# Kernel tuning notes

Hardware: AMD Instinct MI355X
Metric: run time of the kernel (lower is better)

## Reference

```python
import jax, jax.numpy as jnp
import numpy as np

B, L, K1, P = 16, 224, 8192, 16  # batch, spectral bands, pixels, endmembers
LEAKY_SLOPE = 0.01  # torch nn.LeakyReLU default


def setup_inputs() -> dict:
    key = jax.random.key(0)
    ks = jax.random.split(key, 7)
    return {
        "a": jax.random.normal(ks[0], (B, P, K1), jnp.float32),
        "d2": jax.random.normal(ks[1], (B, P, K1), jnp.float32),
        "y": jax.random.normal(ks[2], (B, L, K1), jnp.float32),
        "w3_w": jax.random.normal(ks[3], (P, P), jnp.float32) * 0.1,  # Conv1d(P,P,1) weight squeezed
        "b3_w": jax.random.normal(ks[4], (P, P), jnp.float32) * 0.1,
        "w3_c": jax.random.normal(ks[5], (1, L, P), jnp.float32),     # kernel codebook
        "sigma": jnp.ones((1,), jnp.float32) * 2.0,
        "ca_w": jax.random.normal(ks[6], (2, P), jnp.float32) * 0.1,  # CA Conv1d(P,2,1) weight squeezed
    }


def reference(a, d2, y, w3_w, b3_w, w3_c, sigma, ca_w):
    # h2 = Conv1d(P,P,1)(a - d2)  -> pointwise matmul over channel dim
    h2 = jnp.einsum('pq,bqn->bpn', w3_w, a - d2)  # (B,P,K1)

    # GaussianKernelLayer: pairwise L2 distances between y pixels (B,L,K1)
    # and codebook columns w3_c (1,L,P), via the GEMM identity
    # ||u-v||^2 = ||u||^2 + ||v||^2 - 2 u.v  (avoids the (B,L,K1,P) broadcast).
    y_sq = jnp.sum(y * y, axis=1)            # (B,K1)
    c_sq = jnp.sum(w3_c * w3_c, axis=1)      # (1,P)
    cross = jnp.einsum('blk,olp->bkp', y, w3_c)  # (B,K1,P)
    dist_sq = jnp.maximum(y_sq[:, :, None] + c_sq[:, None, :] - 2.0 * cross, 0.0)
    dist = jnp.sqrt(dist_sq)                 # (B,K1,P)
    h3 = jnp.exp(-0.5 * jnp.square(dist / sigma[0]))
    h3 = jnp.transpose(h3, (0, 2, 1))        # (B,P,K1)

    # CA channel attention: avg/max pool over pixels -> Conv1d(P,2,1) -> LeakyReLU -> softmax
    avg = jnp.mean(h3, axis=-1)              # (B,P)
    mx = jnp.max(h3, axis=-1)                # (B,P)
    conv_lrelu = lambda v: jax.nn.leaky_relu(jnp.einsum('cp,bp->bc', ca_w, v), LEAKY_SLOPE)
    ratio = jax.nn.softmax(conv_lrelu(avg) + conv_lrelu(mx), axis=-1)  # (B,2)

    # combine center pixel + mean pixel via bmm with ratio
    mid = h3[:, :, K1 // 2]                  # (B,P)
    mean = jnp.mean(h3, axis=-1)             # (B,P)
    stacked = jnp.stack([mid, mean], axis=1)  # (B,2,P)
    comb = jnp.einsum('bc,bcp->bp', ratio, stacked)  # (B,P)

    # h4 = Conv1d(P,P,1)(comb[:, :, None])
    h4 = jnp.einsum('pq,bq->bp', b3_w, comb)[:, :, None]  # (B,P,1)

    return h4 + h2  # broadcast over pixel dim -> (B,P,K1)
```

## Files before the change

### kernel.cpp

```cpp
#include <hip/hip_runtime.h>

#define Bn  16
#define Ln  224
#define K1n 8192
#define Pn  16
#define NCHUNK 32


__global__ __launch_bounds__(256) void k_stats(
    const float* __restrict__ y,
    const float* __restrict__ w3c,
    const float* __restrict__ sigma,
    float* __restrict__ ws_sum,
    float* __restrict__ ws_max,
    float* __restrict__ ws_mid)
{
    __shared__ float s_csq_part[16][Pn];
    __shared__ float s_csq[Pn];
    __shared__ float s_part_s[4][Pn];
    __shared__ float s_part_m[4][Pn];

    const int tid   = threadIdx.x;
    const int b     = blockIdx.x >> 5;
    const int chunk = blockIdx.x & 31;
    const int k     = (chunk << 8) + tid;

    {
        const int p   = tid & 15;
        const int sub = tid >> 4;
        float cs = 0.f;
#pragma unroll
        for (int l = sub; l < Ln; l += 16) {
            float v = w3c[l * Pn + p];
            cs = fmaf(v, v, cs);
        }
        s_csq_part[sub][p] = cs;
    }
    __syncthreads();
    if (tid < Pn) {
        float cs = 0.f;
#pragma unroll
        for (int s = 0; s < 16; ++s) cs += s_csq_part[s][tid];
        s_csq[tid] = cs;
    }
    __syncthreads();

    float cross[Pn];
#pragma unroll
    for (int p = 0; p < Pn; ++p) cross[p] = 0.f;
    float ysq = 0.f;

    const float* yp = y + (size_t)b * Ln * K1n + k;
#pragma unroll 16
    for (int l = 0; l < Ln; ++l) {
        float v = yp[(size_t)l * K1n];
        ysq = fmaf(v, v, ysq);
        const float* wrow = w3c + l * Pn;
#pragma unroll
        for (int p = 0; p < Pn; ++p) cross[p] = fmaf(v, wrow[p], cross[p]);
    }

    const float sg = sigma[0];
    const float nh = -0.5f / (sg * sg);

    float h3[Pn];
#pragma unroll
    for (int p = 0; p < Pn; ++p) {
        float d = fmaxf(ysq + s_csq[p] - 2.f * cross[p], 0.f);
        h3[p] = __expf(d * nh);
    }

    if (k == (K1n / 2)) {
#pragma unroll
        for (int p = 0; p < Pn; ++p) ws_mid[b * Pn + p] = h3[p];
    }

    const int lane = tid & 63;
    const int wv   = tid >> 6;
#pragma unroll
    for (int p = 0; p < Pn; ++p) {
        float s = h3[p];
        float m = h3[p];
#pragma unroll
        for (int off = 32; off > 0; off >>= 1) {
            s += __shfl_down(s, off, 64);
            m = fmaxf(m, __shfl_down(m, off, 64));
        }
        if (lane == 0) { s_part_s[wv][p] = s; s_part_m[wv][p] = m; }
    }
    __syncthreads();
    if (tid < Pn) {
        float s = s_part_s[0][tid] + s_part_s[1][tid] + s_part_s[2][tid] + s_part_s[3][tid];
        float m = fmaxf(fmaxf(s_part_m[0][tid], s_part_m[1][tid]),
                        fmaxf(s_part_m[2][tid], s_part_m[3][tid]));
        const int base = (b * NCHUNK + chunk) * Pn + tid;
        ws_sum[base] = s;
        ws_max[base] = m;
    }
}

__global__ __launch_bounds__(256) void k_out(
    const float* __restrict__ a,
    const float* __restrict__ d2,
    const float* __restrict__ w3w,
    const float* __restrict__ b3w,
    const float* __restrict__ caw,
    const float* __restrict__ ws_sum,
    const float* __restrict__ ws_max,
    const float* __restrict__ ws_mid,
    float* __restrict__ out)
{
    __shared__ float s_w3w[Pn][Pn];
    __shared__ float s_red_s[16][Pn];
    __shared__ float s_red_m[16][Pn];
    __shared__ float s_avg[Pn], s_mx[Pn], s_mid[Pn], s_comb[Pn], s_h4[Pn];
    __shared__ float s_t[2];

    const int tid = threadIdx.x;
    const int b   = blockIdx.x >> 5;
    const int k   = ((blockIdx.x & 31) << 8) + tid;

    if (tid < Pn * Pn) s_w3w[tid >> 4][tid & 15] = w3w[tid];

    {
        const int p   = tid & 15;
        const int grp = tid >> 4;
        const int i0  = (b * NCHUNK + grp)      * Pn + p;
        const int i1  = (b * NCHUNK + grp + 16) * Pn + p;
        if (grp < 16) {
            s_red_s[grp][p] = ws_sum[i0] + ws_sum[i1];
            s_red_m[grp][p] = fmaxf(ws_max[i0], ws_max[i1]);
        }
    }
    __syncthreads();
    if (tid < Pn) {
        float s = 0.f, m = -1.f;
        for (int g = 0; g < 16; ++g) {
            s += s_red_s[g][tid];
            m = fmaxf(m, s_red_m[g][tid]);
        }
        s_avg[tid] = s * (1.f / (float)K1n);
        s_mx[tid]  = m;
        s_mid[tid] = ws_mid[b * Pn + tid];
    }
    __syncthreads();

    if (tid < 2) {
        float t1 = 0.f, t2 = 0.f;
        for (int p = 0; p < Pn; ++p) {
            float cw = caw[tid * Pn + p];
            t1 = fmaf(cw, s_avg[p], t1);
            t2 = fmaf(cw, s_mx[p],  t2);
        }
        t1 = (t1 > 0.f) ? t1 : 0.01f * t1;
        t2 = (t2 > 0.f) ? t2 : 0.01f * t2;
        s_t[tid] = t1 + t2;
    }
    __syncthreads();

    if (tid < Pn) {
        float t0 = s_t[0], u1 = s_t[1];
        float mt = fmaxf(t0, u1);
        float e0 = __expf(t0 - mt), e1 = __expf(u1 - mt);
        float inv = 1.f / (e0 + e1);
        s_comb[tid] = (e0 * inv) * s_mid[tid] + (e1 * inv) * s_avg[tid];
    }
    __syncthreads();

    if (tid < Pn) {
        float h = 0.f;
        for (int q = 0; q < Pn; ++q) h = fmaf(b3w[tid * Pn + q], s_comb[q], h);
        s_h4[tid] = h;
    }
    __syncthreads();

    const size_t base = (size_t)b * Pn * K1n + (size_t)k;
    float diff[Pn];
#pragma unroll
    for (int q = 0; q < Pn; ++q) {
        float av = a [base + (size_t)q * K1n];
        float dv = d2[base + (size_t)q * K1n];
        diff[q] = av - dv;
    }
#pragma unroll
    for (int p = 0; p < Pn; ++p) {
        float h2 = 0.f;
#pragma unroll
        for (int q = 0; q < Pn; ++q) h2 = fmaf(s_w3w[p][q], diff[q], h2);
        out[base + (size_t)p * K1n] = h2 + s_h4[p];
    }
}

extern "C" void kernel_launch(void* const* d_in, const int* in_sizes, int n_in,
                              void* d_out, int out_size, void* d_ws, size_t ws_size,
                              hipStream_t stream) {
    const float* a     = (const float*)d_in[0];
    const float* d2    = (const float*)d_in[1];
    const float* y     = (const float*)d_in[2];
    const float* w3w   = (const float*)d_in[3];
    const float* b3w   = (const float*)d_in[4];
    const float* w3c   = (const float*)d_in[5];
    const float* sigma = (const float*)d_in[6];
    const float* caw   = (const float*)d_in[7];

    float* ws_sum = (float*)d_ws;
    float* ws_max = ws_sum + Bn * NCHUNK * Pn;
    float* ws_mid = ws_max + Bn * NCHUNK * Pn;

    k_stats<<<dim3(Bn * NCHUNK), dim3(256), 0, stream>>>(
        y, w3c, sigma, ws_sum, ws_max, ws_mid);

    k_out<<<dim3(Bn * NCHUNK), dim3(256), 0, stream>>>(
        a, d2, w3w, b3w, caw, ws_sum, ws_max, ws_mid, (float*)d_out);
}
```

Measured before the change: 214.1 us.

## Process two pixels per thread with float2 loads, readlane weights, and prefetching

Each thread now handles two adjacent pixels using float2 loads in both kernels, which halves the grid to 16 chunks per batch. In the stats kernel, codebook weights are held in wave registers and broadcast with readlane instead of re-read per FMA, and the next group of y rows is software-prefetched. This aims to raise memory-level parallelism and cut redundant weight loads, at the cost of more registers (launch_bounds 256,1) and only 256 blocks, which may leave many CUs idle.

```diff
diff --git a/kernel.cpp b/kernel.cpp
--- a/kernel.cpp
+++ b/kernel.cpp
@@ -4,10 +4,14 @@
 #define Ln  224
 #define K1n 8192
 #define Pn  16
-#define NCHUNK 32
-
-
-__global__ __launch_bounds__(256) void k_stats(
+#define NCHUNK 16
+
+
+__device__ __forceinline__ float readlane_f(float v, int lane) {
+    return __uint_as_float(__builtin_amdgcn_readlane(__float_as_uint(v), lane));
+}
+
+__global__ __launch_bounds__(256, 1) void k_stats(
     const float* __restrict__ y,
     const float* __restrict__ w3c,
     const float* __restrict__ sigma,
@@ -21,9 +25,10 @@
     __shared__ float s_part_m[4][Pn];
 
     const int tid   = threadIdx.x;
-    const int b     = blockIdx.x >> 5;
-    const int chunk = blockIdx.x & 31;
-    const int k     = (chunk << 8) + tid;
+    const int lane  = tid & 63;
+    const int wv    = tid >> 6;
+    const int b     = blockIdx.x >> 4;
+    const int chunk = blockIdx.x & 15;
 
     {
         const int p   = tid & 15;
@@ -45,42 +50,65 @@
     }
     __syncthreads();
 
-    float cross[Pn];
-#pragma unroll
-    for (int p = 0; p < Pn; ++p) cross[p] = 0.f;
-    float ysq = 0.f;
-
-    const float* yp = y + (size_t)b * Ln * K1n + k;
-#pragma unroll 16
-    for (int l = 0; l < Ln; ++l) {
-        float v = yp[(size_t)l * K1n];
-        ysq = fmaf(v, v, ysq);
-        const float* wrow = w3c + l * Pn;
-#pragma unroll
-        for (int p = 0; p < Pn; ++p) cross[p] = fmaf(v, wrow[p], cross[p]);
+    float cross0[Pn], cross1[Pn];
+#pragma unroll
+    for (int p = 0; p < Pn; ++p) { cross0[p] = 0.f; cross1[p] = 0.f; }
+    float ysq0 = 0.f, ysq1 = 0.f;
+
+    const float2* yp2 = reinterpret_cast<const float2*>(
+                            y + (size_t)b * Ln * K1n + (chunk << 9)) + tid;
+
+    float2 v[8], vn[8];
+    float wqa = w3c[lane], wqb = w3c[64 + lane], wqan, wqbn;
+#pragma unroll
+    for (int j = 0; j < 8; ++j) v[j] = yp2[(size_t)j * (K1n / 2)];
+
+    for (int g = 0; g < Ln / 8; ++g) {
+        if (g < Ln / 8 - 1) {
+            wqan = w3c[(g + 1) * 128 + lane];
+            wqbn = w3c[(g + 1) * 128 + 64 + lane];
+#pragma unroll
+            for (int j = 0; j < 8; ++j)
+                vn[j] = yp2[(size_t)((g + 1) * 8 + j) * (K1n / 2)];
+        }
+#pragma unroll
+        for (int j = 0; j < 8; ++j) {
+            const float wreg = (j < 4) ? wqa : wqb;
+            ysq0 = fmaf(v[j].x, v[j].x, ysq0);
+            ysq1 = fmaf(v[j].y, v[j].y, ysq1);
+#pragma unroll
+            for (int p = 0; p < Pn; ++p) {
+                float w = readlane_f(wreg, (j & 3) * 16 + p);
+                cross0[p] = fmaf(v[j].x, w, cross0[p]);
+                cross1[p] = fmaf(v[j].y, w, cross1[p]);
+            }
+        }
+        wqa = wqan; wqb = wqbn;
+#pragma unroll
+        for (int j = 0; j < 8; ++j) v[j] = vn[j];
     }
 
     const float sg = sigma[0];
     const float nh = -0.5f / (sg * sg);
 
-    float h3[Pn];
+    float h3e[Pn], h3o[Pn];
 #pragma unroll
     for (int p = 0; p < Pn; ++p) {
-        float d = fmaxf(ysq + s_csq[p] - 2.f * cross[p], 0.f);
-        h3[p] = __expf(d * nh);
-    }
-
-    if (k == (K1n / 2)) {
-#pragma unroll
-        for (int p = 0; p < Pn; ++p) ws_mid[b * Pn + p] = h3[p];
-    }
-
-    const int lane = tid & 63;
-    const int wv   = tid >> 6;
+        float de = fmaxf(ysq0 + s_csq[p] - 2.f * cross0[p], 0.f);
+        float dd = fmaxf(ysq1 + s_csq[p] - 2.f * cross1[p], 0.f);
+        h3e[p] = __expf(de * nh);
+        h3o[p] = __expf(dd * nh);
+    }
+
+    if (chunk == 8 && tid == 0) {
+#pragma unroll
+        for (int p = 0; p < Pn; ++p) ws_mid[b * Pn + p] = h3e[p];
+    }
+
 #pragma unroll
     for (int p = 0; p < Pn; ++p) {
-        float s = h3[p];
-        float m = h3[p];
+        float s = h3e[p] + h3o[p];
+        float m = fmaxf(h3e[p], h3o[p]);
 #pragma unroll
         for (int off = 32; off > 0; off >>= 1) {
             s += __shfl_down(s, off, 64);
@@ -99,7 +127,7 @@
     }
 }
 
-__global__ __launch_bounds__(256) void k_out(
+__global__ __launch_bounds__(256, 1) void k_out(
     const float* __restrict__ a,
     const float* __restrict__ d2,
     const float* __restrict__ w3w,
@@ -117,24 +145,22 @@
     __shared__ float s_t[2];
 
     const int tid = threadIdx.x;
-    const int b   = blockIdx.x >> 5;
-    const int k   = ((blockIdx.x & 31) << 8) + tid;
+    const int b   = blockIdx.x >> 4;
+    const int kb  = (blockIdx.x & 15) << 9;
 
     if (tid < Pn * Pn) s_w3w[tid >> 4][tid & 15] = w3w[tid];
 
     {
         const int p   = tid & 15;
         const int grp = tid >> 4;
-        const int i0  = (b * NCHUNK + grp)      * Pn + p;
-        const int i1  = (b * NCHUNK + grp + 16) * Pn + p;
-        if (grp < 16) {
-            s_red_s[grp][p] = ws_sum[i0] + ws_sum[i1];
-            s_red_m[grp][p] = fmaxf(ws_max[i0], ws_max[i1]);
-        }
+        const int i0  = (b * NCHUNK + grp) * Pn + p;
+        s_red_s[grp][p] = ws_sum[i0];
+        s_red_m[grp][p] = ws_max[i0];
     }
     __syncthreads();
     if (tid < Pn) {
         float s = 0.f, m = -1.f;
+#pragma unroll
         for (int g = 0; g < 16; ++g) {
             s += s_red_s[g][tid];
             m = fmaxf(m, s_red_m[g][tid]);
@@ -174,20 +200,36 @@
     }
     __syncthreads();
 
-    const size_t base = (size_t)b * Pn * K1n + (size_t)k;
-    float diff[Pn];
+    const float2* a2 = reinterpret_cast<const float2*>(
+                           a  + (size_t)b * Pn * K1n + kb) + tid;
+    const float2* d22 = reinterpret_cast<const float2*>(
+                           d2 + (size_t)b * Pn * K1n + kb) + tid;
+    float2* o2 = reinterpret_cast<float2*>(
+                           out + (size_t)b * Pn * K1n + kb) + tid;
+
+    float2 av[Pn], dv[Pn];
+#pragma unroll
+    for (int q = 0; q < Pn; ++q) av[q] = a2 [(size_t)q * (K1n / 2)];
+#pragma unroll
+    for (int q = 0; q < Pn; ++q) dv[q] = d22[(size_t)q * (K1n / 2)];
+
+    float2 diff[Pn];
 #pragma unroll
     for (int q = 0; q < Pn; ++q) {
-        float av = a [base + (size_t)q * K1n];
-        float dv = d2[base + (size_t)q * K1n];
-        diff[q] = av - dv;
+        diff[q].x = av[q].x - dv[q].x;
+        diff[q].y = av[q].y - dv[q].y;
     }
 #pragma unroll
     for (int p = 0; p < Pn; ++p) {
-        float h2 = 0.f;
-#pragma unroll
-        for (int q = 0; q < Pn; ++q) h2 = fmaf(s_w3w[p][q], diff[q], h2);
-        out[base + (size_t)p * K1n] = h2 + s_h4[p];
+        float2 h2;
+        h2.x = h2.y = s_h4[p];
+#pragma unroll
+        for (int q = 0; q < Pn; ++q) {
+            const float w = s_w3w[p][q];
+            h2.x = fmaf(w, diff[q].x, h2.x);
+            h2.y = fmaf(w, diff[q].y, h2.y);
+        }
+        o2[(size_t)p * (K1n / 2)] = h2;
     }
 }
 
```

Result: faster. 208.9 us (-2.5%).

## Double-buffer y through LDS with async loads and vectorize output kernel

Applied to the files above, without the earlier changes.

The stats kernel now streams y into shared memory in 32-band chunks using global_load_lds async copies with double buffering. It keeps codebook weights in registers and broadcasts them with readlane instead of reloading them per band. The output kernel processes two pixels per thread with float2 loads and stores on half as many blocks, with the bias folded into the accumulator init. This trades more LDS use and lower occupancy for better memory-level parallelism and fewer scalar loads.

```diff
diff --git a/kernel.cpp b/kernel.cpp
--- a/kernel.cpp
+++ b/kernel.cpp
@@ -5,7 +5,18 @@
 #define K1n 8192
 #define Pn  16
 #define NCHUNK 32
-
+#define CHR 32
+
+
+__device__ __forceinline__ float readlane_f(float v, int lane) {
+    return __uint_as_float(__builtin_amdgcn_readlane(__float_as_uint(v), lane));
+}
+
+__device__ __forceinline__ void async_copy_16(const float* g, float* l) {
+    __builtin_amdgcn_global_load_lds(
+        (const __attribute__((address_space(1))) unsigned int*)g,
+        (__attribute__((address_space(3))) unsigned int*)l, 16, 0, 0);
+}
 
 __global__ __launch_bounds__(256) void k_stats(
     const float* __restrict__ y,
@@ -15,15 +26,17 @@
     float* __restrict__ ws_max,
     float* __restrict__ ws_mid)
 {
+    __shared__ float s_y[2][CHR][256];
     __shared__ float s_csq_part[16][Pn];
     __shared__ float s_csq[Pn];
     __shared__ float s_part_s[4][Pn];
     __shared__ float s_part_m[4][Pn];
 
     const int tid   = threadIdx.x;
+    const int lane  = tid & 63;
+    const int wv    = tid >> 6;
     const int b     = blockIdx.x >> 5;
     const int chunk = blockIdx.x & 31;
-    const int k     = (chunk << 8) + tid;
 
     {
         const int p   = tid & 15;
@@ -43,21 +56,46 @@
         for (int s = 0; s < 16; ++s) cs += s_csq_part[s][tid];
         s_csq[tid] = cs;
     }
-    __syncthreads();
 
     float cross[Pn];
 #pragma unroll
     for (int p = 0; p < Pn; ++p) cross[p] = 0.f;
     float ysq = 0.f;
 
-    const float* yp = y + (size_t)b * Ln * K1n + k;
-#pragma unroll 16
-    for (int l = 0; l < Ln; ++l) {
-        float v = yp[(size_t)l * K1n];
-        ysq = fmaf(v, v, ysq);
-        const float* wrow = w3c + l * Pn;
-#pragma unroll
-        for (int p = 0; p < Pn; ++p) cross[p] = fmaf(v, wrow[p], cross[p]);
+    const float* ysrc = y + (size_t)b * Ln * K1n + (chunk << 8) + (lane << 2);
+
+    float wq[8], wqn[8];
+#pragma unroll
+    for (int i = 0; i < 8; ++i) wq[i] = w3c[i * 64 + lane];
+
+    for (int r = wv; r < CHR; r += 4)
+        async_copy_16(ysrc + (size_t)r * K1n, &s_y[0][r][0]);
+    __syncthreads();
+
+    for (int c = 0; c < Ln / CHR; ++c) {
+        const int cb = c & 1;
+        if (c < Ln / CHR - 1) {
+            for (int r = wv; r < CHR; r += 4)
+                async_copy_16(ysrc + (size_t)((c + 1) * CHR + r) * K1n,
+                              &s_y[cb ^ 1][r][0]);
+#pragma unroll
+            for (int i = 0; i < 8; ++i)
+                wqn[i] = w3c[(c + 1) * (CHR * Pn) + i * 64 + lane];
+        }
+#pragma unroll
+        for (int i = 0; i < 8; ++i) {
+#pragma unroll
+            for (int j = 0; j < 4; ++j) {
+                float v = s_y[cb][i * 4 + j][tid];
+                ysq = fmaf(v, v, ysq);
+#pragma unroll
+                for (int p = 0; p < Pn; ++p)
+                    cross[p] = fmaf(v, readlane_f(wq[i], j * 16 + p), cross[p]);
+            }
+        }
+#pragma unroll
+        for (int i = 0; i < 8; ++i) wq[i] = wqn[i];
+        __syncthreads();
     }
 
     const float sg = sigma[0];
@@ -70,13 +108,11 @@
         h3[p] = __expf(d * nh);
     }
 
-    if (k == (K1n / 2)) {
+    if (chunk == 16 && tid == 0) {
 #pragma unroll
         for (int p = 0; p < Pn; ++p) ws_mid[b * Pn + p] = h3[p];
     }
 
-    const int lane = tid & 63;
-    const int wv   = tid >> 6;
 #pragma unroll
     for (int p = 0; p < Pn; ++p) {
         float s = h3[p];
@@ -99,7 +135,7 @@
     }
 }
 
-__global__ __launch_bounds__(256) void k_out(
+__global__ __launch_bounds__(256, 1) void k_out(
     const float* __restrict__ a,
     const float* __restrict__ d2,
     const float* __restrict__ w3w,
@@ -117,8 +153,8 @@
     __shared__ float s_t[2];
 
     const int tid = threadIdx.x;
-    const int b   = blockIdx.x >> 5;
-    const int k   = ((blockIdx.x & 31) << 8) + tid;
+    const int b   = blockIdx.x >> 4;
+    const int kb  = (blockIdx.x & 15) << 9;
 
     if (tid < Pn * Pn) s_w3w[tid >> 4][tid & 15] = w3w[tid];
 
@@ -127,14 +163,13 @@
         const int grp = tid >> 4;
         const int i0  = (b * NCHUNK + grp)      * Pn + p;
         const int i1  = (b * NCHUNK + grp + 16) * Pn + p;
-        if (grp < 16) {
-            s_red_s[grp][p] = ws_sum[i0] + ws_sum[i1];
-            s_red_m[grp][p] = fmaxf(ws_max[i0], ws_max[i1]);
-        }
+        s_red_s[grp][p] = ws_sum[i0] + ws_sum[i1];
+        s_red_m[grp][p] = fmaxf(ws_max[i0], ws_max[i1]);
     }
     __syncthreads();
     if (tid < Pn) {
         float s = 0.f, m = -1.f;
+#pragma unroll
         for (int g = 0; g < 16; ++g) {
             s += s_red_s[g][tid];
             m = fmaxf(m, s_red_m[g][tid]);
@@ -174,20 +209,36 @@
     }
     __syncthreads();
 
-    const size_t base = (size_t)b * Pn * K1n + (size_t)k;
-    float diff[Pn];
+    const float2* a2  = reinterpret_cast<const float2*>(
+                            a  + (size_t)b * Pn * K1n + kb) + tid;
+    const float2* d22 = reinterpret_cast<const float2*>(
+                            d2 + (size_t)b * Pn * K1n + kb) + tid;
+    float2* o2 = reinterpret_cast<float2*>(
+                            out + (size_t)b * Pn * K1n + kb) + tid;
+
+    float2 av[Pn], dv[Pn];
+#pragma unroll
+    for (int q = 0; q < Pn; ++q) av[q] = a2 [(size_t)q * (K1n / 2)];
+#pragma unroll
+    for (int q = 0; q < Pn; ++q) dv[q] = d22[(size_t)q * (K1n / 2)];
+
+    float2 diff[Pn];
 #pragma unroll
     for (int q = 0; q < Pn; ++q) {
-        float av = a [base + (size_t)q * K1n];
-        float dv = d2[base + (size_t)q * K1n];
-        diff[q] = av - dv;
+        diff[q].x = av[q].x - dv[q].x;
+        diff[q].y = av[q].y - dv[q].y;
     }
 #pragma unroll
     for (int p = 0; p < Pn; ++p) {
-        float h2 = 0.f;
-#pragma unroll
-        for (int q = 0; q < Pn; ++q) h2 = fmaf(s_w3w[p][q], diff[q], h2);
-        out[base + (size_t)p * K1n] = h2 + s_h4[p];
+        float2 h2;
+        h2.x = h2.y = s_h4[p];
+#pragma unroll
+        for (int q = 0; q < Pn; ++q) {
+            const float w = s_w3w[p][q];
+            h2.x = fmaf(w, diff[q].x, h2.x);
+            h2.y = fmaf(w, diff[q].y, h2.y);
+        }
+        o2[(size_t)p * (K1n / 2)] = h2;
     }
 }
 
@@ -210,6 +261,6 @@
     k_stats<<<dim3(Bn * NCHUNK), dim3(256), 0, stream>>>(
         y, w3c, sigma, ws_sum, ws_max, ws_mid);
 
-    k_out<<<dim3(Bn * NCHUNK), dim3(256), 0, stream>>>(
+    k_out<<<dim3(Bn * (K1n / 512)), dim3(256), 0, stream>>>(
         a, d2, w3w, b3w, caw, ws_sum, ws_max, ws_mid, (float*)d_out);
 }
```

Result: no change. 215.6 us (+0.7%).
